# Performance work log

Measured on AMD Instinct MI355X. Metric: run time of the kernel, lower is better.

## Reference

```python
import jax, jax.numpy as jnp
import numpy as np

N_NODES = 50000
N_EDGES = 1600000
N_GRAPHS = 256
IN_CH = 128
HID = 128
OUT_CH = 10


def gcn_conv(x, W, b, src, dst, ew, num_nodes):
    # PyG GCNConv: add self-loops (weight 1), symmetric deg^-1/2 normalization,
    # linear transform first, aggregate via scatter-add, bias after.
    loop = jnp.arange(num_nodes)
    s = jnp.concatenate([src, loop])
    d = jnp.concatenate([dst, loop])
    w = jnp.concatenate([ew, jnp.ones((num_nodes,), x.dtype)])
    deg = jax.ops.segment_sum(w, d, num_segments=num_nodes)
    dinv = jnp.where(deg > 0, jax.lax.rsqrt(deg), 0.0)
    norm = dinv[s] * dinv[d] * w                     # [E+N]
    h = x @ W                                        # [N, H]
    msg = h[s] * norm[:, None]                       # gather + scale
    out = jax.ops.segment_sum(msg, d, num_segments=num_nodes)  # scatter-add
    return out + b


def setup_inputs() -> dict:
    key = jax.random.key(0)
    ks = jax.random.split(key, 12)
    x = jax.random.normal(ks[0], (N_NODES, IN_CH), jnp.float32)
    edge_index = jax.random.randint(ks[1], (2, N_EDGES), 0, N_NODES, jnp.int64)
    edge_weight = jax.random.uniform(ks[2], (N_EDGES,), jnp.float32)
    batch = jnp.sort(jax.random.randint(ks[3], (N_NODES,), 0, N_GRAPHS, jnp.int64))
    s = 1.0 / np.sqrt(HID)
    W1 = jax.random.normal(ks[4], (IN_CH, HID), jnp.float32) / np.sqrt(IN_CH)
    b1 = jnp.zeros((HID,), jnp.float32)
    W2 = jax.random.normal(ks[5], (HID, HID), jnp.float32) * s
    b2 = jnp.zeros((HID,), jnp.float32)
    W3 = jax.random.normal(ks[6], (HID, HID), jnp.float32) * s
    b3 = jnp.zeros((HID,), jnp.float32)
    lw1 = jax.random.normal(ks[7], (HID, HID), jnp.float32) * s
    lb1 = jax.random.normal(ks[8], (HID,), jnp.float32) * s
    lw2 = jax.random.normal(ks[9], (HID, OUT_CH), jnp.float32) * s
    lb2 = jax.random.normal(ks[10], (OUT_CH,), jnp.float32) * s
    return {"x": x, "edge_index": edge_index, "edge_weight": edge_weight,
            "batch": batch, "W1": W1, "b1": b1, "W2": W2, "b2": b2,
            "W3": W3, "b3": b3, "lw1": lw1, "lb1": lb1, "lw2": lw2, "lb2": lb2}


def reference(x, edge_index, edge_weight, batch, W1, b1, W2, b2, W3, b3, lw1, lb1, lw2, lb2):
    src, dst = edge_index[0], edge_index[1]
    h = jax.nn.relu(gcn_conv(x, W1, b1, src, dst, edge_weight, N_NODES))
    h = jax.nn.relu(gcn_conv(h, W2, b2, src, dst, edge_weight, N_NODES))
    h = gcn_conv(h, W3, b3, src, dst, edge_weight, N_NODES)
    # global mean pool over graphs
    sums = jax.ops.segment_sum(h, batch, num_segments=N_GRAPHS)
    cnt = jax.ops.segment_sum(jnp.ones((N_NODES,), h.dtype), batch, num_segments=N_GRAPHS)
    emb = sums / jnp.maximum(cnt, 1.0)[:, None]      # [G, HID]
    out = (emb @ lw1 + lb1) @ lw2 + lb2              # classify: lin1 -> lin2
    return out
```

## Files before the change

kernel.cpp:

```cpp
#include <hip/hip_runtime.h>

#define N_NODES 50000
#define N_EDGES 1600000
#define N_GRAPHS 256
#define HID 128
#define OUT_CH 10
#define PAD 80
#define NBUCK 512
#define BNODES ((N_NODES + NBUCK - 1) / NBUCK)
#define BCAP 6144
#define P1BLK 250
#define EPB (N_EDGES / P1BLK)
#define DSENTINEL 127

typedef __bf16 bf16x8 __attribute__((ext_vector_type(8)));
typedef float f32x4 __attribute__((ext_vector_type(4)));

__device__ inline unsigned bf16rne(float f) {
    unsigned u = __float_as_uint(f);
    return (u + 0x7fffu + ((u >> 16) & 1u)) >> 16;
}

__global__ __launch_bounds__(1024) void bucket_k(const int* __restrict__ src,
                                                 const int* __restrict__ dst,
                                                 const float* __restrict__ ew,
                                                 int* __restrict__ bcount,
                                                 int2* __restrict__ cpair) {
    __shared__ int hist[NBUCK];
    __shared__ int base[NBUCK];
    int t = threadIdx.x;
    for (int i = t; i < NBUCK; i += 1024) hist[i] = 0;
    __syncthreads();
    const int ch0 = blockIdx.x * (EPB / 4);
    const int ch1 = ch0 + (EPB / 4);
    const int4* dst4 = (const int4*)dst;
    for (int ci = ch0 + t; ci < ch1; ci += 1024) {
        int4 d4 = dst4[ci];
        atomicAdd(&hist[d4.x / BNODES], 1);
        atomicAdd(&hist[d4.y / BNODES], 1);
        atomicAdd(&hist[d4.z / BNODES], 1);
        atomicAdd(&hist[d4.w / BNODES], 1);
    }
    __syncthreads();
    for (int i = t; i < NBUCK; i += 1024) {
        int c = hist[i];
        base[i] = (c > 0) ? atomicAdd(&bcount[i], (c + 7) & ~7) : 0;
        hist[i] = 0;
    }
    __syncthreads();
    for (int ci = ch0 + t; ci < ch1; ci += 1024) {
        int4 d4 = dst4[ci];
        int e = ci * 4;
#define PROC(dd, ee)                                              \
        {                                                         \
            int b = (dd) / BNODES;                                \
            int off = base[b] + atomicAdd(&hist[b], 1);           \
            if (off < BCAP) {                                     \
                int2 p;                                           \
                p.x = (((dd) - b * BNODES) << 16) | src[ee];      \
                p.y = __float_as_int(ew[ee]);                     \
                cpair[b * BCAP + off] = p;                        \
            }                                                     \
        }
        PROC(d4.x, e)
        PROC(d4.y, e + 1)
        PROC(d4.z, e + 2)
        PROC(d4.w, e + 3)
#undef PROC
    }
    __syncthreads();
    for (int i = t; i < NBUCK; i += 1024) {
        int c = hist[i];
        int ac = (c + 7) & ~7;
        for (int j = c; j < ac; ++j) {
            int off = base[i] + j;
            if (off < BCAP) {
                int2 p;
                p.x = DSENTINEL << 16;
                p.y = 0;
                cpair[i * BCAP + off] = p;
            }
        }
    }
}

__global__ __launch_bounds__(512) void ell_scatter_k(const int* __restrict__ bcount,
                                                     const int2* __restrict__ cpair,
                                                     int2* __restrict__ ell,
                                                     int* __restrict__ fill,
                                                     float* __restrict__ dinv) {
    __shared__ int lfill[BNODES];
    __shared__ float wsum[BNODES];
    int b = blockIdx.x;
    int t = threadIdx.x;
    for (int i = t; i < BNODES; i += 512) {
        lfill[i] = 0;
        wsum[i] = 0.f;
    }
    __syncthreads();
    int cnt = bcount[b];
    if (cnt > BCAP) cnt = BCAP;
    int n0 = b * BNODES;
    int sbase = b * BCAP;
    for (int i = t; i < cnt; i += 512) {
        int2 p = cpair[sbase + i];
        int dloc = p.x >> 16;
        if (dloc < BNODES) {
            int pos = atomicAdd(&lfill[dloc], 1);
            atomicAdd(&wsum[dloc], __int_as_float(p.y));
            if (pos < PAD) {
                int2 q;
                q.x = p.x & 0xffff;
                q.y = p.y;
                ell[(size_t)(n0 + dloc) * PAD + pos] = q;
            }
        }
    }
    __syncthreads();
    for (int i = t; i < BNODES; i += 512) {
        int n = n0 + i;
        if (n < N_NODES) {
            fill[n] = lfill[i] < PAD ? lfill[i] : PAD;
            dinv[n] = rsqrtf(wsum[i] + 1.0f);
        }
    }
}

__global__ __launch_bounds__(256) void scale_k(int2* __restrict__ ell,
                                               const int* __restrict__ fill,
                                               const float* __restrict__ dinv) {
    int idx = blockIdx.x * blockDim.x + threadIdx.x;
    if (idx >= N_NODES * PAD) return;
    int n = idx / PAD;
    int j = idx - n * PAD;
    if (j < fill[n]) {
        int2 p = ell[idx];
        p.y = __float_as_int(__int_as_float(p.y) * dinv[p.x] * dinv[n]);
        ell[idx] = p;
    }
}

__global__ __launch_bounds__(256) void prep_k(const int* __restrict__ batch,
                                              int* __restrict__ gstart,
                                              const float* __restrict__ W1,
                                              const float* __restrict__ W2,
                                              const float* __restrict__ W3,
                                              unsigned short* __restrict__ Wt) {
    int idx = blockIdx.x * 256 + threadIdx.x;
    if (idx < 3 * 16384) {
        int m = idx >> 14;
        int r = idx & 16383;
        const float* W = (m == 0) ? W1 : (m == 1) ? W2 : W3;
        int c = r >> 7, k = r & 127;
        Wt[idx] = (unsigned short)bf16rne(W[k * 128 + c]);
    }
    if (idx < N_NODES) {
        int b = batch[idx];
        int bprev = (idx == 0) ? -1 : batch[idx - 1];
        for (int g = bprev + 1; g <= b; ++g) gstart[g] = idx;
        if (idx == N_NODES - 1) {
            for (int g = b + 1; g <= N_GRAPHS; ++g) gstart[g] = N_NODES;
        }
    }
}

__global__ __launch_bounds__(256) void gemm_mfma_k(const float* __restrict__ A32,
                                                   const unsigned short* __restrict__ Ab,
                                                   const unsigned short* __restrict__ Wt,
                                                   unsigned short* __restrict__ Cb,
                                                   int n_rows) {
    int tid = threadIdx.x;
    int wave = tid >> 6;
    int lane = tid & 63;
    int m = lane & 15;
    int quad = lane >> 4;
    int row = blockIdx.x * 64 + wave * 16 + m;
    int rowc = row < n_rows ? row : n_rows - 1;
    f32x4 acc[8] = {};
#pragma unroll
    for (int kc = 0; kc < 4; ++kc) {
        bf16x8 a;
        if (A32) {
            const float4* Ar = (const float4*)(A32 + (size_t)rowc * 128 + kc * 32 + quad * 8);
            float4 lo = Ar[0], hi = Ar[1];
            union { bf16x8 v; unsigned short s[8]; } u;
            u.s[0] = (unsigned short)bf16rne(lo.x);
            u.s[1] = (unsigned short)bf16rne(lo.y);
            u.s[2] = (unsigned short)bf16rne(lo.z);
            u.s[3] = (unsigned short)bf16rne(lo.w);
            u.s[4] = (unsigned short)bf16rne(hi.x);
            u.s[5] = (unsigned short)bf16rne(hi.y);
            u.s[6] = (unsigned short)bf16rne(hi.z);
            u.s[7] = (unsigned short)bf16rne(hi.w);
            a = u.v;
        } else {
            a = *(const bf16x8*)(Ab + (size_t)rowc * 128 + kc * 32 + quad * 8);
        }
#pragma unroll
        for (int ct = 0; ct < 8; ++ct) {
            bf16x8 b = *(const bf16x8*)(Wt + (size_t)(ct * 16 + m) * 128 + kc * 32 + quad * 8);
            acc[ct] = __builtin_amdgcn_mfma_f32_16x16x32_bf16(a, b, acc[ct], 0, 0, 0);
        }
    }
    int obase = blockIdx.x * 64 + wave * 16 + quad * 4;
#pragma unroll
    for (int ct = 0; ct < 8; ++ct) {
#pragma unroll
        for (int r = 0; r < 4; ++r) {
            int n = obase + r;
            if (n < n_rows)
                Cb[(size_t)n * 128 + ct * 16 + m] = (unsigned short)bf16rne(acc[ct][r]);
        }
    }
}

__global__ __launch_bounds__(256) void agg_k(const unsigned short* __restrict__ tb,
                                             const int* __restrict__ fill,
                                             const int2* __restrict__ ell,
                                             const float* __restrict__ dinv,
                                             const float* __restrict__ bias,
                                             unsigned short* __restrict__ outB, int relu) {
    int lane = threadIdx.x & 15;
    int local = threadIdx.x >> 4;
    int n = blockIdx.x * 16 + local;
    if (n >= N_NODES) return;
    float di = dinv[n];
    float sw = di * di;
#define UNP(q, f)                                                 \
    float f##0 = __uint_as_float((q).x << 16);                    \
    float f##1 = __uint_as_float((q).x & 0xffff0000u);            \
    float f##2 = __uint_as_float((q).y << 16);                    \
    float f##3 = __uint_as_float((q).y & 0xffff0000u);            \
    float f##4 = __uint_as_float((q).z << 16);                    \
    float f##5 = __uint_as_float((q).z & 0xffff0000u);            \
    float f##6 = __uint_as_float((q).w << 16);                    \
    float f##7 = __uint_as_float((q).w & 0xffff0000u);
    uint4 qs = ((const uint4*)(tb + (size_t)n * 128))[lane];
    UNP(qs, s)
    float acc0 = s0 * sw, acc1 = s1 * sw, acc2 = s2 * sw, acc3 = s3 * sw;
    float acc4 = s4 * sw, acc5 = s5 * sw, acc6 = s6 * sw, acc7 = s7 * sw;
    const int2* ep = ell + n * PAD;
    int c = fill[n];
    int i = 0;
    for (; i + 4 <= c; i += 4) {
        int2 p0 = ep[i], p1 = ep[i + 1], p2 = ep[i + 2], p3 = ep[i + 3];
        uint4 q0 = ((const uint4*)(tb + (size_t)p0.x * 128))[lane];
        uint4 q1 = ((const uint4*)(tb + (size_t)p1.x * 128))[lane];
        uint4 q2 = ((const uint4*)(tb + (size_t)p2.x * 128))[lane];
        uint4 q3 = ((const uint4*)(tb + (size_t)p3.x * 128))[lane];
        float w0 = __int_as_float(p0.y), w1 = __int_as_float(p1.y);
        float w2 = __int_as_float(p2.y), w3 = __int_as_float(p3.y);
        UNP(q0, a)
        UNP(q1, b)
        UNP(q2, cc)
        UNP(q3, d)
        acc0 += a0 * w0 + b0 * w1 + cc0 * w2 + d0 * w3;
        acc1 += a1 * w0 + b1 * w1 + cc1 * w2 + d1 * w3;
        acc2 += a2 * w0 + b2 * w1 + cc2 * w2 + d2 * w3;
        acc3 += a3 * w0 + b3 * w1 + cc3 * w2 + d3 * w3;
        acc4 += a4 * w0 + b4 * w1 + cc4 * w2 + d4 * w3;
        acc5 += a5 * w0 + b5 * w1 + cc5 * w2 + d5 * w3;
        acc6 += a6 * w0 + b6 * w1 + cc6 * w2 + d6 * w3;
        acc7 += a7 * w0 + b7 * w1 + cc7 * w2 + d7 * w3;
    }
    for (; i < c; ++i) {
        int2 p = ep[i];
        float w = __int_as_float(p.y);
        uint4 q = ((const uint4*)(tb + (size_t)p.x * 128))[lane];
        UNP(q, a)
        acc0 += a0 * w; acc1 += a1 * w; acc2 += a2 * w; acc3 += a3 * w;
        acc4 += a4 * w; acc5 += a5 * w; acc6 += a6 * w; acc7 += a7 * w;
    }
#undef UNP
    float4 b0 = ((const float4*)bias)[lane * 2];
    float4 b1 = ((const float4*)bias)[lane * 2 + 1];
    acc0 += b0.x; acc1 += b0.y; acc2 += b0.z; acc3 += b0.w;
    acc4 += b1.x; acc5 += b1.y; acc6 += b1.z; acc7 += b1.w;
    if (relu) {
        acc0 = fmaxf(acc0, 0.f); acc1 = fmaxf(acc1, 0.f);
        acc2 = fmaxf(acc2, 0.f); acc3 = fmaxf(acc3, 0.f);
        acc4 = fmaxf(acc4, 0.f); acc5 = fmaxf(acc5, 0.f);
        acc6 = fmaxf(acc6, 0.f); acc7 = fmaxf(acc7, 0.f);
    }
    uint4 pk;
    pk.x = bf16rne(acc0) | (bf16rne(acc1) << 16);
    pk.y = bf16rne(acc2) | (bf16rne(acc3) << 16);
    pk.z = bf16rne(acc4) | (bf16rne(acc5) << 16);
    pk.w = bf16rne(acc6) | (bf16rne(acc7) << 16);
    ((uint4*)(outB + (size_t)n * 128))[lane] = pk;
}

#define PCHUNK 49
__global__ __launch_bounds__(128) void pool1_k(const unsigned short* __restrict__ hb,
                                               const int* __restrict__ batch,
                                               float* __restrict__ pool) {
    int c = threadIdx.x;
    int n0 = blockIdx.x * PCHUNK;
    if (n0 >= N_NODES) return;
    int n1 = n0 + PCHUNK;
    if (n1 > N_NODES) n1 = N_NODES;
    int g = batch[n0];
    float run = 0.f;
    for (int n = n0; n < n1; ++n) {
        int gn = batch[n];
        if (gn != g) {
            atomicAdd(&pool[g * 128 + c], run);
            run = 0.f;
            g = gn;
        }
        run += __uint_as_float((unsigned)hb[(size_t)n * 128 + c] << 16);
    }
    atomicAdd(&pool[g * 128 + c], run);
}

__global__ __launch_bounds__(128) void cls2_k(const float* __restrict__ pool,
                                              const int* __restrict__ gstart,
                                              const float* __restrict__ lw1,
                                              const float* __restrict__ lb1,
                                              const float* __restrict__ lw2,
                                              const float* __restrict__ lb2,
                                              float* __restrict__ out) {
    __shared__ float emb[128];
    __shared__ float mid[128];
    int g = blockIdx.x, c = threadIdx.x;
    float cntf = fmaxf((float)(gstart[g + 1] - gstart[g]), 1.0f);
    emb[c] = pool[(size_t)g * 128 + c] / cntf;
    __syncthreads();
    float a = lb1[c];
    for (int k = 0; k < 128; ++k) a += emb[k] * lw1[k * 128 + c];
    mid[c] = a;
    __syncthreads();
    if (c < OUT_CH) {
        float o = lb2[c];
        for (int k = 0; k < 128; ++k) o += mid[k] * lw2[k * OUT_CH + c];
        out[g * OUT_CH + c] = o;
    }
}

extern "C" void kernel_launch(void* const* d_in, const int* in_sizes, int n_in,
                              void* d_out, int out_size, void* d_ws, size_t ws_size,
                              hipStream_t stream) {
    const float* x = (const float*)d_in[0];
    const int* ei = (const int*)d_in[1];
    const int* src = ei;
    const int* dst = ei + N_EDGES;
    const float* ew = (const float*)d_in[2];
    const int* batch = (const int*)d_in[3];
    const float* W1 = (const float*)d_in[4];
    const float* b1 = (const float*)d_in[5];
    const float* W2 = (const float*)d_in[6];
    const float* b2 = (const float*)d_in[7];
    const float* W3 = (const float*)d_in[8];
    const float* b3 = (const float*)d_in[9];
    const float* lw1 = (const float*)d_in[10];
    const float* lb1 = (const float*)d_in[11];
    const float* lw2 = (const float*)d_in[12];
    const float* lb2 = (const float*)d_in[13];
    float* out = (float*)d_out;

    char* ws = (char*)d_ws;
    size_t off = 0;
    auto alloc = [&](size_t bytes) {
        size_t cur = off;
        off += (bytes + 255) & ~(size_t)255;
        return cur;
    };
    size_t o_bcount = alloc(NBUCK * 4);
    size_t o_pool = alloc(N_GRAPHS * HID * 4);
    size_t zero_end = off;
    size_t o_fill = alloc(N_NODES * 4);
    size_t o_dinv = alloc(N_NODES * 4);
    size_t o_gstart = alloc((N_GRAPHS + 1) * 4);
    size_t o_wt = alloc(3 * 16384 * 2);
    size_t o_ell = alloc((size_t)N_NODES * PAD * 8);
    size_t o_cpair = alloc((size_t)NBUCK * BCAP * 8);
    size_t o_gAb = alloc((size_t)N_NODES * HID * 2);
    size_t o_aggB = alloc((size_t)N_NODES * HID * 2);
    (void)ws_size;

    int* bcount = (int*)(ws + o_bcount);
    float* pool = (float*)(ws + o_pool);
    int* fill = (int*)(ws + o_fill);
    float* dinv = (float*)(ws + o_dinv);
    int* gstart = (int*)(ws + o_gstart);
    unsigned short* Wt = (unsigned short*)(ws + o_wt);
    int2* ell = (int2*)(ws + o_ell);
    int2* cpair = (int2*)(ws + o_cpair);
    unsigned short* gAb = (unsigned short*)(ws + o_gAb);
    unsigned short* aggB = (unsigned short*)(ws + o_aggB);

    hipMemsetAsync(d_ws, 0, zero_end, stream);

    bucket_k<<<P1BLK, 1024, 0, stream>>>(src, dst, ew, bcount, cpair);
    ell_scatter_k<<<NBUCK, 512, 0, stream>>>(bcount, cpair, ell, fill, dinv);
    scale_k<<<(N_NODES * PAD + 255) / 256, 256, 0, stream>>>(ell, fill, dinv);
    prep_k<<<196, 256, 0, stream>>>(batch, gstart, W1, W2, W3, Wt);

    int gemm_blocks = (N_NODES + 63) / 64;
    int agg_blocks = (N_NODES + 15) / 16;
    gemm_mfma_k<<<gemm_blocks, 256, 0, stream>>>(x, (const unsigned short*)0, Wt, gAb, N_NODES);
    agg_k<<<agg_blocks, 256, 0, stream>>>(gAb, fill, ell, dinv, b1, aggB, 1);
    gemm_mfma_k<<<gemm_blocks, 256, 0, stream>>>((const float*)0, aggB, Wt + 16384, gAb, N_NODES);
    agg_k<<<agg_blocks, 256, 0, stream>>>(gAb, fill, ell, dinv, b2, aggB, 1);
    gemm_mfma_k<<<gemm_blocks, 256, 0, stream>>>((const float*)0, aggB, Wt + 32768, gAb, N_NODES);
    agg_k<<<agg_blocks, 256, 0, stream>>>(gAb, fill, ell, dinv, b3, aggB, 0);

    pool1_k<<<(N_NODES + PCHUNK - 1) / PCHUNK, 128, 0, stream>>>(aggB, batch, pool);
    cls2_k<<<N_GRAPHS, 128, 0, stream>>>(pool, gstart, lw1, lb1, lw2, lb2, out);
}
```

Measured before the change: 402.5 us.

## Split ELL neighbor lists by source range and fold normalization into aggregation

Each destination's ELL row is split into four sub-lists by source-node range, 40 slots each, with per-range counts packed into one 32-bit word. The aggregation kernel walks the ranges in order, so gathers from source rows stay within a quarter of the feature table at a time, which may improve cache locality. The separate scale kernel is removed. Normalization is applied inside aggregation instead, by multiplying by dinv[src] per edge and by dinv[dst] once at the end. This adds a dinv gather per edge in each of the three layers, and the per-range cap of 40 could drop edges for skewed nodes where the old cap was 80 overall.

Result: faster. 385.7 us (-4.2%).

```diff
diff --git a/kernel.cpp b/kernel.cpp
--- a/kernel.cpp
+++ b/kernel.cpp
@@ -5,13 +5,15 @@
 #define N_GRAPHS 256
 #define HID 128
 #define OUT_CH 10
-#define PAD 80
 #define NBUCK 512
 #define BNODES ((N_NODES + NBUCK - 1) / NBUCK)
 #define BCAP 6144
 #define P1BLK 250
 #define EPB (N_EDGES / P1BLK)
 #define DSENTINEL 127
+#define NR 4
+#define RSTEP ((N_NODES + NR - 1) / NR)
+#define PAD_R 40
 
 typedef __bf16 bf16x8 __attribute__((ext_vector_type(8)));
 typedef float f32x4 __attribute__((ext_vector_type(4)));
@@ -87,16 +89,14 @@
 __global__ __launch_bounds__(512) void ell_scatter_k(const int* __restrict__ bcount,
                                                      const int2* __restrict__ cpair,
                                                      int2* __restrict__ ell,
-                                                     int* __restrict__ fill,
+                                                     unsigned* __restrict__ fill4,
                                                      float* __restrict__ dinv) {
-    __shared__ int lfill[BNODES];
+    __shared__ int lfill[BNODES * NR];
     __shared__ float wsum[BNODES];
     int b = blockIdx.x;
     int t = threadIdx.x;
-    for (int i = t; i < BNODES; i += 512) {
-        lfill[i] = 0;
-        wsum[i] = 0.f;
-    }
+    for (int i = t; i < BNODES * NR; i += 512) lfill[i] = 0;
+    for (int i = t; i < BNODES; i += 512) wsum[i] = 0.f;
     __syncthreads();
     int cnt = bcount[b];
     if (cnt > BCAP) cnt = BCAP;
@@ -106,13 +106,15 @@
         int2 p = cpair[sbase + i];
         int dloc = p.x >> 16;
         if (dloc < BNODES) {
-            int pos = atomicAdd(&lfill[dloc], 1);
+            int s = p.x & 0xffff;
+            int r = s / RSTEP;
+            int pos = atomicAdd(&lfill[dloc * NR + r], 1);
             atomicAdd(&wsum[dloc], __int_as_float(p.y));
-            if (pos < PAD) {
+            if (pos < PAD_R) {
                 int2 q;
-                q.x = p.x & 0xffff;
+                q.x = s;
                 q.y = p.y;
-                ell[(size_t)(n0 + dloc) * PAD + pos] = q;
+                ell[((size_t)(n0 + dloc) * NR + r) * PAD_R + pos] = q;
             }
         }
     }
@@ -120,23 +122,16 @@
     for (int i = t; i < BNODES; i += 512) {
         int n = n0 + i;
         if (n < N_NODES) {
-            fill[n] = lfill[i] < PAD ? lfill[i] : PAD;
+            unsigned f = 0;
+#pragma unroll
+            for (int r = 0; r < NR; ++r) {
+                int c = lfill[i * NR + r];
+                if (c > PAD_R) c = PAD_R;
+                f |= (unsigned)c << (8 * r);
+            }
+            fill4[n] = f;
             dinv[n] = rsqrtf(wsum[i] + 1.0f);
         }
-    }
-}
-
-__global__ __launch_bounds__(256) void scale_k(int2* __restrict__ ell,
-                                               const int* __restrict__ fill,
-                                               const float* __restrict__ dinv) {
-    int idx = blockIdx.x * blockDim.x + threadIdx.x;
-    if (idx >= N_NODES * PAD) return;
-    int n = idx / PAD;
-    int j = idx - n * PAD;
-    if (j < fill[n]) {
-        int2 p = ell[idx];
-        p.y = __float_as_int(__int_as_float(p.y) * dinv[p.x] * dinv[n]);
-        ell[idx] = p;
     }
 }
 
@@ -215,7 +210,7 @@
 }
 
 __global__ __launch_bounds__(256) void agg_k(const unsigned short* __restrict__ tb,
-                                             const int* __restrict__ fill,
+                                             const unsigned* __restrict__ fill4,
                                              const int2* __restrict__ ell,
                                              const float* __restrict__ dinv,
                                              const float* __restrict__ bias,
@@ -224,8 +219,7 @@
     int local = threadIdx.x >> 4;
     int n = blockIdx.x * 16 + local;
     if (n >= N_NODES) return;
-    float di = dinv[n];
-    float sw = di * di;
+    float dn = dinv[n];
 #define UNP(q, f)                                                 \
     float f##0 = __uint_as_float((q).x << 16);                    \
     float f##1 = __uint_as_float((q).x & 0xffff0000u);            \
@@ -237,45 +231,53 @@
     float f##7 = __uint_as_float((q).w & 0xffff0000u);
     uint4 qs = ((const uint4*)(tb + (size_t)n * 128))[lane];
     UNP(qs, s)
-    float acc0 = s0 * sw, acc1 = s1 * sw, acc2 = s2 * sw, acc3 = s3 * sw;
-    float acc4 = s4 * sw, acc5 = s5 * sw, acc6 = s6 * sw, acc7 = s7 * sw;
-    const int2* ep = ell + n * PAD;
-    int c = fill[n];
-    int i = 0;
-    for (; i + 4 <= c; i += 4) {
-        int2 p0 = ep[i], p1 = ep[i + 1], p2 = ep[i + 2], p3 = ep[i + 3];
-        uint4 q0 = ((const uint4*)(tb + (size_t)p0.x * 128))[lane];
-        uint4 q1 = ((const uint4*)(tb + (size_t)p1.x * 128))[lane];
-        uint4 q2 = ((const uint4*)(tb + (size_t)p2.x * 128))[lane];
-        uint4 q3 = ((const uint4*)(tb + (size_t)p3.x * 128))[lane];
-        float w0 = __int_as_float(p0.y), w1 = __int_as_float(p1.y);
-        float w2 = __int_as_float(p2.y), w3 = __int_as_float(p3.y);
-        UNP(q0, a)
-        UNP(q1, b)
-        UNP(q2, cc)
-        UNP(q3, d)
-        acc0 += a0 * w0 + b0 * w1 + cc0 * w2 + d0 * w3;
-        acc1 += a1 * w0 + b1 * w1 + cc1 * w2 + d1 * w3;
-        acc2 += a2 * w0 + b2 * w1 + cc2 * w2 + d2 * w3;
-        acc3 += a3 * w0 + b3 * w1 + cc3 * w2 + d3 * w3;
-        acc4 += a4 * w0 + b4 * w1 + cc4 * w2 + d4 * w3;
-        acc5 += a5 * w0 + b5 * w1 + cc5 * w2 + d5 * w3;
-        acc6 += a6 * w0 + b6 * w1 + cc6 * w2 + d6 * w3;
-        acc7 += a7 * w0 + b7 * w1 + cc7 * w2 + d7 * w3;
-    }
-    for (; i < c; ++i) {
-        int2 p = ep[i];
-        float w = __int_as_float(p.y);
-        uint4 q = ((const uint4*)(tb + (size_t)p.x * 128))[lane];
-        UNP(q, a)
-        acc0 += a0 * w; acc1 += a1 * w; acc2 += a2 * w; acc3 += a3 * w;
-        acc4 += a4 * w; acc5 += a5 * w; acc6 += a6 * w; acc7 += a7 * w;
+    float acc0 = s0 * dn, acc1 = s1 * dn, acc2 = s2 * dn, acc3 = s3 * dn;
+    float acc4 = s4 * dn, acc5 = s5 * dn, acc6 = s6 * dn, acc7 = s7 * dn;
+    unsigned f4 = fill4[n];
+#pragma unroll
+    for (int r = 0; r < NR; ++r) {
+        int c = (f4 >> (8 * r)) & 255;
+        const int2* ep = ell + ((size_t)n * NR + r) * PAD_R;
+        int i = 0;
+        for (; i + 4 <= c; i += 4) {
+            int2 p0 = ep[i], p1 = ep[i + 1], p2 = ep[i + 2], p3 = ep[i + 3];
+            uint4 q0 = ((const uint4*)(tb + (size_t)p0.x * 128))[lane];
+            uint4 q1 = ((const uint4*)(tb + (size_t)p1.x * 128))[lane];
+            uint4 q2 = ((const uint4*)(tb + (size_t)p2.x * 128))[lane];
+            uint4 q3 = ((const uint4*)(tb + (size_t)p3.x * 128))[lane];
+            float w0 = __int_as_float(p0.y) * dinv[p0.x];
+            float w1 = __int_as_float(p1.y) * dinv[p1.x];
+            float w2 = __int_as_float(p2.y) * dinv[p2.x];
+            float w3 = __int_as_float(p3.y) * dinv[p3.x];
+            UNP(q0, a)
+            UNP(q1, b)
+            UNP(q2, cc)
+            UNP(q3, d)
+            acc0 += a0 * w0 + b0 * w1 + cc0 * w2 + d0 * w3;
+            acc1 += a1 * w0 + b1 * w1 + cc1 * w2 + d1 * w3;
+            acc2 += a2 * w0 + b2 * w1 + cc2 * w2 + d2 * w3;
+            acc3 += a3 * w0 + b3 * w1 + cc3 * w2 + d3 * w3;
+            acc4 += a4 * w0 + b4 * w1 + cc4 * w2 + d4 * w3;
+            acc5 += a5 * w0 + b5 * w1 + cc5 * w2 + d5 * w3;
+            acc6 += a6 * w0 + b6 * w1 + cc6 * w2 + d6 * w3;
+            acc7 += a7 * w0 + b7 * w1 + cc7 * w2 + d7 * w3;
+        }
+        for (; i < c; ++i) {
+            int2 p = ep[i];
+            float w = __int_as_float(p.y) * dinv[p.x];
+            uint4 q = ((const uint4*)(tb + (size_t)p.x * 128))[lane];
+            UNP(q, a)
+            acc0 += a0 * w; acc1 += a1 * w; acc2 += a2 * w; acc3 += a3 * w;
+            acc4 += a4 * w; acc5 += a5 * w; acc6 += a6 * w; acc7 += a7 * w;
+        }
     }
 #undef UNP
     float4 b0 = ((const float4*)bias)[lane * 2];
     float4 b1 = ((const float4*)bias)[lane * 2 + 1];
-    acc0 += b0.x; acc1 += b0.y; acc2 += b0.z; acc3 += b0.w;
-    acc4 += b1.x; acc5 += b1.y; acc6 += b1.z; acc7 += b1.w;
+    acc0 = acc0 * dn + b0.x; acc1 = acc1 * dn + b0.y;
+    acc2 = acc2 * dn + b0.z; acc3 = acc3 * dn + b0.w;
+    acc4 = acc4 * dn + b1.x; acc5 = acc5 * dn + b1.y;
+    acc6 = acc6 * dn + b1.z; acc7 = acc7 * dn + b1.w;
     if (relu) {
         acc0 = fmaxf(acc0, 0.f); acc1 = fmaxf(acc1, 0.f);
         acc2 = fmaxf(acc2, 0.f); acc3 = fmaxf(acc3, 0.f);
@@ -368,11 +370,11 @@
     size_t o_bcount = alloc(NBUCK * 4);
     size_t o_pool = alloc(N_GRAPHS * HID * 4);
     size_t zero_end = off;
-    size_t o_fill = alloc(N_NODES * 4);
+    size_t o_fill4 = alloc(N_NODES * 4);
     size_t o_dinv = alloc(N_NODES * 4);
     size_t o_gstart = alloc((N_GRAPHS + 1) * 4);
     size_t o_wt = alloc(3 * 16384 * 2);
-    size_t o_ell = alloc((size_t)N_NODES * PAD * 8);
+    size_t o_ell = alloc((size_t)N_NODES * NR * PAD_R * 8);
     size_t o_cpair = alloc((size_t)NBUCK * BCAP * 8);
     size_t o_gAb = alloc((size_t)N_NODES * HID * 2);
     size_t o_aggB = alloc((size_t)N_NODES * HID * 2);
@@ -380,7 +382,7 @@
 
     int* bcount = (int*)(ws + o_bcount);
     float* pool = (float*)(ws + o_pool);
-    int* fill = (int*)(ws + o_fill);
+    unsigned* fill4 = (unsigned*)(ws + o_fill4);
     float* dinv = (float*)(ws + o_dinv);
     int* gstart = (int*)(ws + o_gstart);
     unsigned short* Wt = (unsigned short*)(ws + o_wt);
@@ -392,18 +394,17 @@
     hipMemsetAsync(d_ws, 0, zero_end, stream);
 
     bucket_k<<<P1BLK, 1024, 0, stream>>>(src, dst, ew, bcount, cpair);
-    ell_scatter_k<<<NBUCK, 512, 0, stream>>>(bcount, cpair, ell, fill, dinv);
-    scale_k<<<(N_NODES * PAD + 255) / 256, 256, 0, stream>>>(ell, fill, dinv);
+    ell_scatter_k<<<NBUCK, 512, 0, stream>>>(bcount, cpair, ell, fill4, dinv);
     prep_k<<<196, 256, 0, stream>>>(batch, gstart, W1, W2, W3, Wt);
 
     int gemm_blocks = (N_NODES + 63) / 64;
     int agg_blocks = (N_NODES + 15) / 16;
     gemm_mfma_k<<<gemm_blocks, 256, 0, stream>>>(x, (const unsigned short*)0, Wt, gAb, N_NODES);
-    agg_k<<<agg_blocks, 256, 0, stream>>>(gAb, fill, ell, dinv, b1, aggB, 1);
+    agg_k<<<agg_blocks, 256, 0, stream>>>(gAb, fill4, ell, dinv, b1, aggB, 1);
     gemm_mfma_k<<<gemm_blocks, 256, 0, stream>>>((const float*)0, aggB, Wt + 16384, gAb, N_NODES);
-    agg_k<<<agg_blocks, 256, 0, stream>>>(gAb, fill, ell, dinv, b2, aggB, 1);
+    agg_k<<<agg_blocks, 256, 0, stream>>>(gAb, fill4, ell, dinv, b2, aggB, 1);
     gemm_mfma_k<<<gemm_blocks, 256, 0, stream>>>((const float*)0, aggB, Wt + 32768, gAb, N_NODES);
-    agg_k<<<agg_blocks, 256, 0, stream>>>(gAb, fill, ell, dinv, b3, aggB, 0);
+    agg_k<<<agg_blocks, 256, 0, stream>>>(gAb, fill4, ell, dinv, b3, aggB, 0);
 
     pool1_k<<<(N_NODES + PCHUNK - 1) / PCHUNK, 128, 0, stream>>>(aggB, batch, pool);
     cls2_k<<<N_GRAPHS, 128, 0, stream>>>(pool, gstart, lw1, lb1, lw2, lb2, out);
```

## Split node features into column chunks and fold normalization into aggregation

Applied to the files above, without the earlier changes.

Stores intermediate node features as four column-chunked planes of 32 bf16 values each, so every aggregation block gathers only 64-byte rows from one chunk. The working set per pass is smaller and more cache-friendly for the random neighbor gathers. The separate scale kernel that pre-multiplied edge weights by dinv is removed; dinv of the source is instead applied per edge inside aggregation and dinv of the destination once at the end. The cost is four times more reads of the ELL index and dinv, smaller 8-byte per-lane loads, and scattered GEMM output stores.

After: 479.3 us. 19.1% more time.

```diff
diff --git a/kernel.cpp b/kernel.cpp
--- a/kernel.cpp
+++ b/kernel.cpp
@@ -12,6 +12,8 @@
 #define P1BLK 250
 #define EPB (N_EDGES / P1BLK)
 #define DSENTINEL 127
+#define NCHUNK 4
+#define CCH 32
 
 typedef __bf16 bf16x8 __attribute__((ext_vector_type(8)));
 typedef float f32x4 __attribute__((ext_vector_type(4)));
@@ -123,20 +125,6 @@
             fill[n] = lfill[i] < PAD ? lfill[i] : PAD;
             dinv[n] = rsqrtf(wsum[i] + 1.0f);
         }
-    }
-}
-
-__global__ __launch_bounds__(256) void scale_k(int2* __restrict__ ell,
-                                               const int* __restrict__ fill,
-                                               const float* __restrict__ dinv) {
-    int idx = blockIdx.x * blockDim.x + threadIdx.x;
-    if (idx >= N_NODES * PAD) return;
-    int n = idx / PAD;
-    int j = idx - n * PAD;
-    if (j < fill[n]) {
-        int2 p = ell[idx];
-        p.y = __float_as_int(__int_as_float(p.y) * dinv[p.x] * dinv[n]);
-        ell[idx] = p;
     }
 }
 
@@ -194,7 +182,7 @@
             u.s[7] = (unsigned short)bf16rne(hi.w);
             a = u.v;
         } else {
-            a = *(const bf16x8*)(Ab + (size_t)rowc * 128 + kc * 32 + quad * 8);
+            a = *(const bf16x8*)(Ab + ((size_t)kc * N_NODES + rowc) * CCH + quad * 8);
         }
 #pragma unroll
         for (int ct = 0; ct < 8; ++ct) {
@@ -205,11 +193,13 @@
     int obase = blockIdx.x * 64 + wave * 16 + quad * 4;
 #pragma unroll
     for (int ct = 0; ct < 8; ++ct) {
+        int col = ct * 16 + m;
+        size_t cbase = ((size_t)(col >> 5) * N_NODES) * CCH + (col & 31);
 #pragma unroll
         for (int r = 0; r < 4; ++r) {
             int n = obase + r;
             if (n < n_rows)
-                Cb[(size_t)n * 128 + ct * 16 + m] = (unsigned short)bf16rne(acc[ct][r]);
+                Cb[cbase + (size_t)n * CCH] = (unsigned short)bf16rne(acc[ct][r]);
         }
     }
 }
@@ -219,37 +209,37 @@
                                              const int2* __restrict__ ell,
                                              const float* __restrict__ dinv,
                                              const float* __restrict__ bias,
-                                             unsigned short* __restrict__ outB, int relu) {
-    int lane = threadIdx.x & 15;
-    int local = threadIdx.x >> 4;
-    int n = blockIdx.x * 16 + local;
+                                             unsigned short* __restrict__ outB, int relu,
+                                             int blks_per_chunk) {
+    int chunk = blockIdx.x / blks_per_chunk;
+    int nb = blockIdx.x - chunk * blks_per_chunk;
+    int lane = threadIdx.x & 7;
+    int local = threadIdx.x >> 3;
+    int n = nb * 32 + local;
     if (n >= N_NODES) return;
-    float di = dinv[n];
-    float sw = di * di;
+    const unsigned short* tbc = tb + (size_t)chunk * N_NODES * CCH;
+    float dn = dinv[n];
 #define UNP(q, f)                                                 \
     float f##0 = __uint_as_float((q).x << 16);                    \
     float f##1 = __uint_as_float((q).x & 0xffff0000u);            \
     float f##2 = __uint_as_float((q).y << 16);                    \
-    float f##3 = __uint_as_float((q).y & 0xffff0000u);            \
-    float f##4 = __uint_as_float((q).z << 16);                    \
-    float f##5 = __uint_as_float((q).z & 0xffff0000u);            \
-    float f##6 = __uint_as_float((q).w << 16);                    \
-    float f##7 = __uint_as_float((q).w & 0xffff0000u);
-    uint4 qs = ((const uint4*)(tb + (size_t)n * 128))[lane];
+    float f##3 = __uint_as_float((q).y & 0xffff0000u);
+    uint2 qs = *(const uint2*)(tbc + (size_t)n * CCH + lane * 4);
     UNP(qs, s)
-    float acc0 = s0 * sw, acc1 = s1 * sw, acc2 = s2 * sw, acc3 = s3 * sw;
-    float acc4 = s4 * sw, acc5 = s5 * sw, acc6 = s6 * sw, acc7 = s7 * sw;
-    const int2* ep = ell + n * PAD;
+    float acc0 = s0 * dn, acc1 = s1 * dn, acc2 = s2 * dn, acc3 = s3 * dn;
+    const int2* ep = ell + (size_t)n * PAD;
     int c = fill[n];
     int i = 0;
     for (; i + 4 <= c; i += 4) {
         int2 p0 = ep[i], p1 = ep[i + 1], p2 = ep[i + 2], p3 = ep[i + 3];
-        uint4 q0 = ((const uint4*)(tb + (size_t)p0.x * 128))[lane];
-        uint4 q1 = ((const uint4*)(tb + (size_t)p1.x * 128))[lane];
-        uint4 q2 = ((const uint4*)(tb + (size_t)p2.x * 128))[lane];
-        uint4 q3 = ((const uint4*)(tb + (size_t)p3.x * 128))[lane];
-        float w0 = __int_as_float(p0.y), w1 = __int_as_float(p1.y);
-        float w2 = __int_as_float(p2.y), w3 = __int_as_float(p3.y);
+        uint2 q0 = *(const uint2*)(tbc + (size_t)p0.x * CCH + lane * 4);
+        uint2 q1 = *(const uint2*)(tbc + (size_t)p1.x * CCH + lane * 4);
+        uint2 q2 = *(const uint2*)(tbc + (size_t)p2.x * CCH + lane * 4);
+        uint2 q3 = *(const uint2*)(tbc + (size_t)p3.x * CCH + lane * 4);
+        float w0 = __int_as_float(p0.y) * dinv[p0.x];
+        float w1 = __int_as_float(p1.y) * dinv[p1.x];
+        float w2 = __int_as_float(p2.y) * dinv[p2.x];
+        float w3 = __int_as_float(p3.y) * dinv[p3.x];
         UNP(q0, a)
         UNP(q1, b)
         UNP(q2, cc)
@@ -258,36 +248,28 @@
         acc1 += a1 * w0 + b1 * w1 + cc1 * w2 + d1 * w3;
         acc2 += a2 * w0 + b2 * w1 + cc2 * w2 + d2 * w3;
         acc3 += a3 * w0 + b3 * w1 + cc3 * w2 + d3 * w3;
-        acc4 += a4 * w0 + b4 * w1 + cc4 * w2 + d4 * w3;
-        acc5 += a5 * w0 + b5 * w1 + cc5 * w2 + d5 * w3;
-        acc6 += a6 * w0 + b6 * w1 + cc6 * w2 + d6 * w3;
-        acc7 += a7 * w0 + b7 * w1 + cc7 * w2 + d7 * w3;
     }
     for (; i < c; ++i) {
         int2 p = ep[i];
-        float w = __int_as_float(p.y);
-        uint4 q = ((const uint4*)(tb + (size_t)p.x * 128))[lane];
+        float w = __int_as_float(p.y) * dinv[p.x];
+        uint2 q = *(const uint2*)(tbc + (size_t)p.x * CCH + lane * 4);
         UNP(q, a)
         acc0 += a0 * w; acc1 += a1 * w; acc2 += a2 * w; acc3 += a3 * w;
-        acc4 += a4 * w; acc5 += a5 * w; acc6 += a6 * w; acc7 += a7 * w;
     }
 #undef UNP
-    float4 b0 = ((const float4*)bias)[lane * 2];
-    float4 b1 = ((const float4*)bias)[lane * 2 + 1];
-    acc0 += b0.x; acc1 += b0.y; acc2 += b0.z; acc3 += b0.w;
-    acc4 += b1.x; acc5 += b1.y; acc6 += b1.z; acc7 += b1.w;
+    float4 b = ((const float4*)bias)[chunk * 8 + lane];
+    acc0 = acc0 * dn + b.x;
+    acc1 = acc1 * dn + b.y;
+    acc2 = acc2 * dn + b.z;
+    acc3 = acc3 * dn + b.w;
     if (relu) {
         acc0 = fmaxf(acc0, 0.f); acc1 = fmaxf(acc1, 0.f);
         acc2 = fmaxf(acc2, 0.f); acc3 = fmaxf(acc3, 0.f);
-        acc4 = fmaxf(acc4, 0.f); acc5 = fmaxf(acc5, 0.f);
-        acc6 = fmaxf(acc6, 0.f); acc7 = fmaxf(acc7, 0.f);
-    }
-    uint4 pk;
+    }
+    uint2 pk;
     pk.x = bf16rne(acc0) | (bf16rne(acc1) << 16);
     pk.y = bf16rne(acc2) | (bf16rne(acc3) << 16);
-    pk.z = bf16rne(acc4) | (bf16rne(acc5) << 16);
-    pk.w = bf16rne(acc6) | (bf16rne(acc7) << 16);
-    ((uint4*)(outB + (size_t)n * 128))[lane] = pk;
+    *(uint2*)(outB + ((size_t)chunk * N_NODES + n) * CCH + lane * 4) = pk;
 }
 
 #define PCHUNK 49
@@ -295,6 +277,7 @@
                                                const int* __restrict__ batch,
                                                float* __restrict__ pool) {
     int c = threadIdx.x;
+    const unsigned short* hc = hb + (size_t)(c >> 5) * N_NODES * CCH + (c & 31);
     int n0 = blockIdx.x * PCHUNK;
     if (n0 >= N_NODES) return;
     int n1 = n0 + PCHUNK;
@@ -308,7 +291,7 @@
             run = 0.f;
             g = gn;
         }
-        run += __uint_as_float((unsigned)hb[(size_t)n * 128 + c] << 16);
+        run += __uint_as_float((unsigned)hc[(size_t)n * CCH] << 16);
     }
     atomicAdd(&pool[g * 128 + c], run);
 }
@@ -393,17 +376,17 @@
 
     bucket_k<<<P1BLK, 1024, 0, stream>>>(src, dst, ew, bcount, cpair);
     ell_scatter_k<<<NBUCK, 512, 0, stream>>>(bcount, cpair, ell, fill, dinv);
-    scale_k<<<(N_NODES * PAD + 255) / 256, 256, 0, stream>>>(ell, fill, dinv);
     prep_k<<<196, 256, 0, stream>>>(batch, gstart, W1, W2, W3, Wt);
 
     int gemm_blocks = (N_NODES + 63) / 64;
-    int agg_blocks = (N_NODES + 15) / 16;
+    int bpc = (N_NODES + 31) / 32;
+    int agg_blocks = bpc * NCHUNK;
     gemm_mfma_k<<<gemm_blocks, 256, 0, stream>>>(x, (const unsigned short*)0, Wt, gAb, N_NODES);
-    agg_k<<<agg_blocks, 256, 0, stream>>>(gAb, fill, ell, dinv, b1, aggB, 1);
+    agg_k<<<agg_blocks, 256, 0, stream>>>(gAb, fill, ell, dinv, b1, aggB, 1, bpc);
     gemm_mfma_k<<<gemm_blocks, 256, 0, stream>>>((const float*)0, aggB, Wt + 16384, gAb, N_NODES);
-    agg_k<<<agg_blocks, 256, 0, stream>>>(gAb, fill, ell, dinv, b2, aggB, 1);
+    agg_k<<<agg_blocks, 256, 0, stream>>>(gAb, fill, ell, dinv, b2, aggB, 1, bpc);
     gemm_mfma_k<<<gemm_blocks, 256, 0, stream>>>((const float*)0, aggB, Wt + 32768, gAb, N_NODES);
-    agg_k<<<agg_blocks, 256, 0, stream>>>(gAb, fill, ell, dinv, b3, aggB, 0);
+    agg_k<<<agg_blocks, 256, 0, stream>>>(gAb, fill, ell, dinv, b3, aggB, 0, bpc);
 
     pool1_k<<<(N_NODES + PCHUNK - 1) / PCHUNK, 128, 0, stream>>>(aggB, batch, pool);
     cls2_k<<<N_GRAPHS, 128, 0, stream>>>(pool, gstart, lw1, lb1, lw2, lb2, out);
```
